# Performance work log

Hardware: AMD Instinct MI355X
Metric: run time of the kernel (lower is better)

## Reference

```python
import jax, jax.numpy as jnp
import numpy as np

B, S, D = 4, 2048, 512   # batch, seq_len, head_size (== d_model)
H = 8                    # num_heads
DH = D // H              # depth per head = 64


def setup_inputs() -> dict:
    key = jax.random.key(0)
    ks = jax.random.split(key, 11)
    sc = 1.0 / np.sqrt(D)
    inp = {
        "q": jax.random.normal(ks[0], (B, S, D), jnp.float32),
        "k": jax.random.normal(ks[1], (B, S, D), jnp.float32),
        "v": jax.random.normal(ks[2], (B, S, D), jnp.float32),
        # causal mask: 1.0 where attention is disallowed (j > i)
        "mask": jnp.triu(jnp.ones((S, S), jnp.float32), k=1)[None, None, :, :],
        "wq": jax.random.normal(ks[3], (D, D), jnp.float32) * sc,
        "bq": jnp.zeros((D,), jnp.float32),
        "wk": jax.random.normal(ks[4], (D, D), jnp.float32) * sc,
        "bk": jnp.zeros((D,), jnp.float32),
        "wv": jax.random.normal(ks[5], (D, D), jnp.float32) * sc,
        "bv": jnp.zeros((D,), jnp.float32),
        "wo": jax.random.normal(ks[6], (D, D), jnp.float32) * sc,
        "bo": jnp.zeros((D,), jnp.float32),
    }
    return inp


def _split_heads(x):
    # [B,S,D] -> [B,H,S,DH]
    return x.reshape(B, S, H, DH).transpose(0, 2, 1, 3)


def reference(q, k, v, mask, wq, bq, wk, bk, wv, bv, wo, bo):
    query = _split_heads(q @ wq + bq)
    key_h = _split_heads(k @ wk + bk)
    value = _split_heads(v @ wv + bv)

    scale = 1.0 / jnp.sqrt(jnp.asarray(DH, jnp.float32))
    scores = jnp.einsum("bhqd,bhkd->bhqk", query, key_h) * scale
    scores = scores + mask * -1e9
    attn = jax.nn.softmax(scores, axis=-1)  # [B,H,S,S]

    ctx = jnp.einsum("bhqk,bhkd->bhqd", attn, value)
    ctx = ctx.transpose(0, 2, 1, 3).reshape(B, S, D)  # concat heads
    out = ctx @ wo + bo
    return out, attn
```

## Files before the change

### kernel.cpp

```cpp
#include <hip/hip_runtime.h>

#define Bq 4
#define Sq 2048
#define Dq 512
#define Hq 8
#define DHq 64

typedef __attribute__((ext_vector_type(8))) short bf16x8;
typedef __attribute__((ext_vector_type(4))) float floatx4;

__device__ __forceinline__ unsigned short f2bf(float f) {
  union { float f; unsigned u; } v; v.f = f;
  return (unsigned short)((v.u + 0x7fffu + ((v.u >> 16) & 1u)) >> 16);
}

__device__ __forceinline__ void gload16(const unsigned short* g,
                                        unsigned short* l) {
  __builtin_amdgcn_global_load_lds(
      (const __attribute__((address_space(1))) void*)g,
      (__attribute__((address_space(3))) void*)l, 16, 0, 0);
}

__global__ __launch_bounds__(256) void wtrans(
    const float* wq, const float* wk, const float* wv, const float* wo,
    unsigned short* WT) {
  const int wz = blockIdx.y;
  const float* W = (wz == 0) ? wq : (wz == 1) ? wk : (wz == 2) ? wv : wo;
  unsigned short* WTz = WT + (size_t)wz * 512 * 512;
  const int k0 = (blockIdx.x >> 3) << 6;
  const int n0 = (blockIdx.x & 7) << 6;
  const int tid = threadIdx.x;
  __shared__ unsigned short T[64][65];
#pragma unroll
  for (int it = 0; it < 16; ++it) {
    int idx = tid + it * 256;
    int r = idx >> 6, c = idx & 63;
    T[c][r] = f2bf(W[(size_t)(k0 + r) * 512 + n0 + c]);
  }
  __syncthreads();
#pragma unroll
  for (int it = 0; it < 2; ++it) {
    int e = tid + it * 256;
    int n = e >> 3, koct = e & 7;
    union { unsigned short u[8]; uint4 v; } pk;
#pragma unroll
    for (int j = 0; j < 8; ++j) pk.u[j] = T[n][koct * 8 + j];
    *(uint4*)&WTz[(size_t)(n0 + n) * 512 + k0 + koct * 8] = pk.v;
  }
}

template <int MODE>
__global__ __launch_bounds__(256) void gemm_kernel(
    const float* A0, const float* A1, const float* A2,
    const unsigned short* Ab, const unsigned short* WT,
    const float* b0, const float* b1, const float* b2,
    unsigned short* O0, unsigned short* O1, unsigned short* VtO,
    float* Fout) {
  const int bz = blockIdx.z;
  const float* A = (bz == 0) ? A0 : (bz == 1) ? A1 : A2;
  const float* bias = (bz == 0) ? b0 : (bz == 1) ? b1 : b2;
  const unsigned short* WTz = WT + (size_t)((MODE == 1) ? 3 : bz) * 262144;

  const int bm = blockIdx.x;
  const int bn = blockIdx.y;
  const int tid = threadIdx.x;
  const int lane = tid & 63;
  const int w = tid >> 6, wm = w >> 1, wn = w & 1;
  const int lg = lane >> 4, lc = lane & 15;

  __shared__ unsigned short As[4096], Bs[4096];

  floatx4 acc[4][4];
#pragma unroll
  for (int mt = 0; mt < 4; ++mt)
#pragma unroll
    for (int nt = 0; nt < 4; ++nt) acc[mt][nt] = (floatx4){0.f, 0.f, 0.f, 0.f};

  for (int kt = 0; kt < 16; ++kt) {
    __syncthreads();
    if (MODE == 0) {
#pragma unroll
      for (int it = 0; it < 4; ++it) {
        int idx = tid + it * 256;
        int m = idx >> 3, k0 = (idx & 7) << 2;
        const float4 va =
            *(const float4*)(A + (size_t)(bm * 128 + m) * 512 + kt * 32 + k0);
        union { unsigned short u[4]; uint2 v; } pk;
        pk.u[0] = f2bf(va.x); pk.u[1] = f2bf(va.y);
        pk.u[2] = f2bf(va.z); pk.u[3] = f2bf(va.w);
        *(uint2*)&As[(((k0 >> 3) * 128 + m) << 3) + (k0 & 7)] = pk.v;
      }
    } else {
#pragma unroll
      for (int it = 0; it < 2; ++it) {
        int c = tid + it * 256;
        gload16(Ab + (size_t)(bm * 128 + (c & 127)) * 512 + kt * 32 +
                    (c >> 7) * 8,
                &As[c << 3]);
      }
    }
#pragma unroll
    for (int it = 0; it < 2; ++it) {
      int c = tid + it * 256;
      gload16(WTz + (size_t)(bn * 128 + (c & 127)) * 512 + kt * 32 +
                  (c >> 7) * 8,
              &Bs[c << 3]);
    }
    __syncthreads();

    bf16x8 af[4], bfr[4];
#pragma unroll
    for (int mt = 0; mt < 4; ++mt)
      af[mt] = *(const bf16x8*)&As[(lg * 128 + wm * 64 + mt * 16 + lc) << 3];
#pragma unroll
    for (int nt = 0; nt < 4; ++nt)
      bfr[nt] = *(const bf16x8*)&Bs[(lg * 128 + wn * 64 + nt * 16 + lc) << 3];
#pragma unroll
    for (int mt = 0; mt < 4; ++mt)
#pragma unroll
      for (int nt = 0; nt < 4; ++nt)
        acc[mt][nt] = __builtin_amdgcn_mfma_f32_16x16x32_bf16(
            af[mt], bfr[nt], acc[mt][nt], 0, 0, 0);
  }

#pragma unroll
  for (int mt = 0; mt < 4; ++mt) {
#pragma unroll
    for (int nt = 0; nt < 4; ++nt) {
      const int col = bn * 128 + wn * 64 + nt * 16 + lc;
      const float bvv = bias[col];
      const int row0 = bm * 128 + wm * 64 + mt * 16 + lg * 4;
      if (MODE == 1) {
#pragma unroll
        for (int r = 0; r < 4; ++r)
          Fout[(size_t)(row0 + r) * 512 + col] = acc[mt][nt][r] + bvv;
      } else if (bz == 2) {
        union { unsigned short u[4]; uint2 v; } pk;
#pragma unroll
        for (int r = 0; r < 4; ++r) pk.u[r] = f2bf(acc[mt][nt][r] + bvv);
        const int bb = row0 >> 11, s0 = row0 & 2047;
        const int hh = col >> 6, dh = col & 63;
        *(uint2*)&VtO[((size_t)((bb * 8 + hh) * 64 + dh)) * 2048 + s0] = pk.v;
      } else {
        unsigned short* O = (bz == 0) ? O0 : O1;
#pragma unroll
        for (int r = 0; r < 4; ++r)
          O[(size_t)(row0 + r) * 512 + col] = f2bf(acc[mt][nt][r] + bvv);
      }
    }
  }
}

__global__ __launch_bounds__(256) void attn_kernel(
    const unsigned short* __restrict__ Qb, const unsigned short* __restrict__ Kb,
    const unsigned short* __restrict__ Vt, float* __restrict__ attn,
    unsigned short* __restrict__ ctxb) {
  const int lid = blockIdx.x;
  const int xcd = lid & 7;
  const int idx = lid >> 3;
  const int bh = xcd * 4 + (idx >> 5);
  const int qt = idx & 31;
  const int b = bh >> 3, h = bh & 7;

  const int tid = threadIdx.x;
  const int lane = tid & 63, w = tid >> 6;
  const int lg = lane >> 4, lc = lane & 15;
  const int q0 = qt * 64 + w * 16;
  const int qi = q0 + lc;

  __shared__ unsigned short Ps[4096];
  unsigned short* Pw = &Ps[w * 1024];

  bf16x8 bQ[2];
#pragma unroll
  for (int ks = 0; ks < 2; ++ks)
    bQ[ks] = *(const bf16x8*)&Qb[(size_t)(b * Sq + q0 + lc) * Dq + h * DHq +
                                 (ks * 4 + lg) * 8];

  const unsigned short* kb = &Kb[(size_t)(b * Sq) * Dq + h * DHq];
  float mrun = -1e30f, lrun = 0.f;

  for (int jt = 0; jt <= qt; ++jt) {
    const unsigned short* kt_ = kb + (size_t)(jt * 64) * Dq;
    floatx4 s[4];
#pragma unroll
    for (int nt = 0; nt < 4; ++nt) s[nt] = (floatx4){0.f, 0.f, 0.f, 0.f};
#pragma unroll
    for (int ks = 0; ks < 2; ++ks)
#pragma unroll
      for (int nt = 0; nt < 4; ++nt) {
        bf16x8 ak = *(const bf16x8*)&kt_[(size_t)(nt * 16 + lc) * Dq +
                                         (ks * 4 + lg) * 8];
        s[nt] = __builtin_amdgcn_mfma_f32_16x16x32_bf16(ak, bQ[ks], s[nt],
                                                        0, 0, 0);
      }
    float sv[4][4];
    float mx = -1e30f;
    const int kjb = jt * 64 + lg * 4;
#pragma unroll
    for (int nt = 0; nt < 4; ++nt)
#pragma unroll
      for (int r = 0; r < 4; ++r) {
        float x = s[nt][r] * 0.125f;
        if (kjb + nt * 16 + r > qi) x = -1e30f;
        sv[nt][r] = x;
        mx = fmaxf(mx, x);
      }
    mx = fmaxf(mx, __shfl_xor(mx, 16));
    mx = fmaxf(mx, __shfl_xor(mx, 32));
    const float mnew = fmaxf(mrun, mx);
    float sum = 0.f;
#pragma unroll
    for (int nt = 0; nt < 4; ++nt)
#pragma unroll
      for (int r = 0; r < 4; ++r) sum += __expf(sv[nt][r] - mnew);
    sum += __shfl_xor(sum, 16);
    sum += __shfl_xor(sum, 32);
    lrun = lrun * __expf(mrun - mnew) + sum;
    mrun = mnew;
  }
  const float rinv = 1.0f / lrun;

  floatx4 ctxa[4];
#pragma unroll
  for (int nt = 0; nt < 4; ++nt) ctxa[nt] = (floatx4){0.f, 0.f, 0.f, 0.f};
  float* abase = attn + (size_t)(b * Hq + h) * Sq * Sq;
  const unsigned short* vb = &Vt[(size_t)((b * Hq + h) * DHq) * Sq];

  for (int jt = 0; jt <= qt; ++jt) {
    const unsigned short* kt_ = kb + (size_t)(jt * 64) * Dq;
    floatx4 s[4];
#pragma unroll
    for (int nt = 0; nt < 4; ++nt) s[nt] = (floatx4){0.f, 0.f, 0.f, 0.f};
#pragma unroll
    for (int ks = 0; ks < 2; ++ks)
#pragma unroll
      for (int nt = 0; nt < 4; ++nt) {
        bf16x8 ak = *(const bf16x8*)&kt_[(size_t)(nt * 16 + lc) * Dq +
                                         (ks * 4 + lg) * 8];
        s[nt] = __builtin_amdgcn_mfma_f32_16x16x32_bf16(ak, bQ[ks], s[nt],
                                                        0, 0, 0);
      }
    const int kjb = jt * 64 + lg * 4;
#pragma unroll
    for (int nt = 0; nt < 4; ++nt) {
      floatx4 pv;
      union { unsigned short u[4]; uint2 v2; } pb;
#pragma unroll
      for (int r = 0; r < 4; ++r) {
        float x = s[nt][r] * 0.125f;
        float p = (kjb + nt * 16 + r > qi) ? 0.f : __expf(x - mrun) * rinv;
        pv[r] = p;
        pb.u[r] = f2bf(p);
      }
      __builtin_nontemporal_store(
          pv, (floatx4*)&abase[(size_t)qi * Sq + jt * 64 + nt * 16 + lg * 4]);
      *(uint2*)&Pw[((nt * 2 + (lg >> 1)) * 16 + lc) * 8 + (lg & 1) * 4] =
          pb.v2;
    }
    bf16x8 ap[2];
#pragma unroll
    for (int ks = 0; ks < 2; ++ks)
      ap[ks] = *(const bf16x8*)&Pw[((ks * 4 + lg) * 16 + lc) * 8];
#pragma unroll
    for (int ks = 0; ks < 2; ++ks)
#pragma unroll
      for (int nt = 0; nt < 4; ++nt) {
        bf16x8 bv = *(const bf16x8*)&vb[(size_t)(nt * 16 + lc) * Sq + jt * 64 +
                                        (ks * 4 + lg) * 8];
        ctxa[nt] = __builtin_amdgcn_mfma_f32_16x16x32_bf16(ap[ks], bv,
                                                           ctxa[nt], 0, 0, 0);
      }
  }

#pragma unroll
  for (int nt = 0; nt < 4; ++nt)
#pragma unroll
    for (int r = 0; r < 4; ++r)
      ctxb[(size_t)(b * Sq + q0 + lg * 4 + r) * Dq + h * DHq + nt * 16 + lc] =
          f2bf(ctxa[nt][r]);

  const floatx4 z4 = {0.f, 0.f, 0.f, 0.f};
  const int kend = (qt + 1) * 64;
  for (int rr = 0; rr < 16; ++rr) {
    float* rp = abase + (size_t)(q0 + rr) * Sq;
    for (int c = kend + lane * 4; c < Sq; c += 256)
      __builtin_nontemporal_store(z4, (floatx4*)&rp[c]);
  }
}

extern "C" void kernel_launch(void* const* d_in, const int* in_sizes, int n_in,
                              void* d_out, int out_size, void* d_ws,
                              size_t ws_size, hipStream_t stream) {
  const float* q = (const float*)d_in[0];
  const float* k = (const float*)d_in[1];
  const float* v = (const float*)d_in[2];
  const float* wq = (const float*)d_in[4];
  const float* bq = (const float*)d_in[5];
  const float* wk = (const float*)d_in[6];
  const float* bk = (const float*)d_in[7];
  const float* wv = (const float*)d_in[8];
  const float* bv = (const float*)d_in[9];
  const float* wo = (const float*)d_in[10];
  const float* bo = (const float*)d_in[11];

  float* out = (float*)d_out;
  float* attn = out + (size_t)Bq * Sq * Dq;

  unsigned short* Qb = (unsigned short*)d_ws;
  unsigned short* Kb = Qb + (size_t)Bq * Sq * Dq;
  unsigned short* Vt = Kb + (size_t)Bq * Sq * Dq;
  unsigned short* ctxb = Vt + (size_t)Bq * Sq * Dq;
  unsigned short* WTb = ctxb + (size_t)Bq * Sq * Dq;

  dim3 blk(256);
  wtrans<<<dim3(64, 4), blk, 0, stream>>>(wq, wk, wv, wo, WTb);

  gemm_kernel<0><<<dim3(64, 4, 3), blk, 0, stream>>>(
      q, k, v, nullptr, WTb, bq, bk, bv, Qb, Kb, Vt, nullptr);

  attn_kernel<<<dim3(1024, 1, 1), blk, 0, stream>>>(Qb, Kb, Vt, attn, ctxb);

  gemm_kernel<1><<<dim3(64, 4, 1), blk, 0, stream>>>(
      nullptr, nullptr, nullptr, ctxb, WTb, bo, nullptr, nullptr, nullptr,
      nullptr, nullptr, out);
}
```

Baseline: 913.7 us.

## Stage K/V tiles in double-buffered swizzled LDS and reverse query-tile order

```diff
diff --git a/kernel.cpp b/kernel.cpp
--- a/kernel.cpp
+++ b/kernel.cpp
@@ -159,7 +159,7 @@
   const int xcd = lid & 7;
   const int idx = lid >> 3;
   const int bh = xcd * 4 + (idx >> 5);
-  const int qt = idx & 31;
+  const int qt = 31 - (idx & 31);
   const int b = bh >> 3, h = bh & 7;
 
   const int tid = threadIdx.x;
@@ -168,20 +168,47 @@
   const int q0 = qt * 64 + w * 16;
   const int qi = q0 + lc;
 
+  __shared__ unsigned short Ksh[2][4096];
+  __shared__ unsigned short Vsh[2][4096];
   __shared__ unsigned short Ps[4096];
   unsigned short* Pw = &Ps[w * 1024];
 
+  const unsigned short* kb = &Kb[(size_t)(b * Sq) * Dq + h * DHq];
+  const unsigned short* vb = &Vt[(size_t)((b * Hq + h) * DHq) * Sq];
+
+#define STAGE_K(jt_, buf_)                                                    \
+  {                                                                           \
+    _Pragma("unroll") for (int it = 0; it < 2; ++it) {                        \
+      int c = tid + it * 256;                                                 \
+      int row = c >> 3;                                                       \
+      int sc = ((c & 7) ^ (row & 7)) << 3;                                    \
+      gload16(kb + (size_t)((jt_) * 64 + row) * Dq + sc, &Ksh[buf_][c << 3]); \
+    }                                                                         \
+  }
+#define STAGE_V(jt_, buf_)                                                    \
+  {                                                                           \
+    _Pragma("unroll") for (int it = 0; it < 2; ++it) {                        \
+      int c = tid + it * 256;                                                 \
+      int dh = c >> 3;                                                        \
+      int sc = ((c & 7) ^ (dh & 7)) << 3;                                     \
+      gload16(vb + (size_t)dh * Sq + (jt_) * 64 + sc, &Vsh[buf_][c << 3]);    \
+    }                                                                         \
+  }
+
   bf16x8 bQ[2];
 #pragma unroll
   for (int ks = 0; ks < 2; ++ks)
-    bQ[ks] = *(const bf16x8*)&Qb[(size_t)(b * Sq + q0 + lc) * Dq + h * DHq +
+    bQ[ks] = *(const bf16x8*)&Qb[(size_t)(b * Sq + qi) * Dq + h * DHq +
                                  (ks * 4 + lg) * 8];
 
-  const unsigned short* kb = &Kb[(size_t)(b * Sq) * Dq + h * DHq];
   float mrun = -1e30f, lrun = 0.f;
 
+  STAGE_K(0, 0);
   for (int jt = 0; jt <= qt; ++jt) {
-    const unsigned short* kt_ = kb + (size_t)(jt * 64) * Dq;
+    const int cur = jt & 1;
+    __syncthreads();
+    if (jt < qt) STAGE_K(jt + 1, cur ^ 1);
+
     floatx4 s[4];
 #pragma unroll
     for (int nt = 0; nt < 4; ++nt) s[nt] = (floatx4){0.f, 0.f, 0.f, 0.f};
@@ -189,8 +216,9 @@
     for (int ks = 0; ks < 2; ++ks)
 #pragma unroll
       for (int nt = 0; nt < 4; ++nt) {
-        bf16x8 ak = *(const bf16x8*)&kt_[(size_t)(nt * 16 + lc) * Dq +
-                                         (ks * 4 + lg) * 8];
+        const int rk = nt * 16 + lc;
+        bf16x8 ak = *(const bf16x8*)
+            &Ksh[cur][(rk << 6) + ((((ks << 2) + lg) ^ (rk & 7)) << 3)];
         s[nt] = __builtin_amdgcn_mfma_f32_16x16x32_bf16(ak, bQ[ks], s[nt],
                                                         0, 0, 0);
       }
@@ -225,10 +253,15 @@
 #pragma unroll
   for (int nt = 0; nt < 4; ++nt) ctxa[nt] = (floatx4){0.f, 0.f, 0.f, 0.f};
   float* abase = attn + (size_t)(b * Hq + h) * Sq * Sq;
-  const unsigned short* vb = &Vt[(size_t)((b * Hq + h) * DHq) * Sq];
-
+
+  __syncthreads();
+  STAGE_K(0, 0);
+  STAGE_V(0, 0);
   for (int jt = 0; jt <= qt; ++jt) {
-    const unsigned short* kt_ = kb + (size_t)(jt * 64) * Dq;
+    const int cur = jt & 1;
+    __syncthreads();
+    if (jt < qt) { STAGE_K(jt + 1, cur ^ 1); STAGE_V(jt + 1, cur ^ 1); }
+
     floatx4 s[4];
 #pragma unroll
     for (int nt = 0; nt < 4; ++nt) s[nt] = (floatx4){0.f, 0.f, 0.f, 0.f};
@@ -236,8 +269,9 @@
     for (int ks = 0; ks < 2; ++ks)
 #pragma unroll
       for (int nt = 0; nt < 4; ++nt) {
-        bf16x8 ak = *(const bf16x8*)&kt_[(size_t)(nt * 16 + lc) * Dq +
-                                         (ks * 4 + lg) * 8];
+        const int rk = nt * 16 + lc;
+        bf16x8 ak = *(const bf16x8*)
+            &Ksh[cur][(rk << 6) + ((((ks << 2) + lg) ^ (rk & 7)) << 3)];
         s[nt] = __builtin_amdgcn_mfma_f32_16x16x32_bf16(ak, bQ[ks], s[nt],
                                                         0, 0, 0);
       }
@@ -266,8 +300,9 @@
     for (int ks = 0; ks < 2; ++ks)
 #pragma unroll
       for (int nt = 0; nt < 4; ++nt) {
-        bf16x8 bv = *(const bf16x8*)&vb[(size_t)(nt * 16 + lc) * Sq + jt * 64 +
-                                        (ks * 4 + lg) * 8];
+        const int rv = nt * 16 + lc;
+        bf16x8 bv = *(const bf16x8*)
+            &Vsh[cur][(rv << 6) + ((((ks << 2) + lg) ^ (rv & 7)) << 3)];
         ctxa[nt] = __builtin_amdgcn_mfma_f32_16x16x32_bf16(ap[ks], bv,
                                                            ctxa[nt], 0, 0, 0);
       }
@@ -287,6 +322,8 @@
     for (int c = kend + lane * 4; c < Sq; c += 256)
       __builtin_nontemporal_store(z4, (floatx4*)&rp[c]);
   }
+#undef STAGE_K
+#undef STAGE_V
 }
 
 extern "C" void kernel_launch(void* const* d_in, const int* in_sizes, int n_in,
```

Result: faster. 760.3 us (-16.8%).
